# Kernel tuning notes

Measured on AMD Instinct MI355X. Metric: run time of the kernel, lower is better.

The kernel has to match this reference:

```python
import jax, jax.numpy as jnp
import numpy as np

NUM_FREQS = 10
NUM_VOXELS = 512
N_POINTS = 262144
IN_DIM = 3
INPUT_CH = IN_DIM + 2 * NUM_FREQS * IN_DIM  # 63


def posenc(x, num_freqs):
    # NeRF positional encoding: [x, sin(x*2^0), cos(x*2^0), ..., sin(x*2^(F-1)), cos(x*2^(F-1))]
    freqs = (2.0 ** jnp.arange(num_freqs)).astype(x.dtype)           # (F,)
    xf = x[:, None, :] * freqs[None, :, None]                        # (N, F, D)
    sc = jnp.stack([jnp.sin(xf), jnp.cos(xf)], axis=2)               # (N, F, 2, D)
    return jnp.concatenate([x, sc.reshape(x.shape[0], -1)], axis=-1)  # (N, D + 2*F*D)


def setup_inputs() -> dict:
    key = jax.random.key(0)
    k_x, k_w, k_v = jax.random.split(key, 3)
    X = jax.random.normal(k_x, (N_POINTS, IN_DIM), dtype=jnp.float32)
    # linear_mappings reshaped to (3*num_voxels, input_ch), used as Linear weight (no bias)
    W = jax.random.normal(k_w, (3 * NUM_VOXELS, INPUT_CH), dtype=jnp.float32) * 0.02
    row_ids = jnp.arange(N_POINTS, dtype=jnp.int64 if jax.config.jax_enable_x64 else jnp.int32)
    voxel_ids = jax.random.randint(k_v, (N_POINTS,), 0, NUM_VOXELS)
    return {"X": X, "W": W, "row_ids": row_ids, "voxel_ids": voxel_ids}


def reference(X, W, row_ids, voxel_ids):
    encoded_X = posenc(X, NUM_FREQS)                      # (N, 63)
    rgb_clusters = encoded_X @ W.T                        # (N, 3*num_voxels) -- wasteful dense GEMM
    # col_indices per selected row: [3v, 3v+1, 3v+2]
    cols = jnp.stack([3 * voxel_ids, 3 * voxel_ids + 1, 3 * voxel_ids + 2], axis=1)  # (M, 3)
    vals = rgb_clusters[row_ids[:, None], cols]           # (M, 3)
    rgb = jnp.zeros((X.shape[0], 3), dtype=X.dtype)
    rgb = rgb.at[row_ids].set(vals)
    return rgb
```

## Files before the change

### kernel.cpp

```cpp
#include <hip/hip_runtime.h>
#include <math.h>

#define N_POINTS   262144
#define NUM_FREQS  10
#define NUM_VOXELS 512
#define HALF_VOX   256
#define VSTRIDE    200
#define HALF_HALFS (HALF_VOX * VSTRIDE)
#define HALF_F4    (HALF_HALFS / 8)
#define CHUNKS     (HALF_HALFS * 2 / 1024)


typedef _Float16 half2v __attribute__((ext_vector_type(2)));

__device__ __forceinline__ half2v u2h(unsigned int u) {
    union { unsigned int u; half2v h; } c; c.u = u; return c.h;
}

__device__ __forceinline__ float dot2acc(half2v a, half2v b, float acc) {
#if __has_builtin(__builtin_amdgcn_fdot2)
    return __builtin_amdgcn_fdot2(a, b, acc, false);
#else
    return acc + (float)a[0] * (float)b[0] + (float)a[1] * (float)b[1];
#endif
}

__device__ __forceinline__ half2v pkrtz(float a, float b) {
#if __has_builtin(__builtin_amdgcn_cvt_pkrtz)
    auto r = __builtin_amdgcn_cvt_pkrtz(a, b);
    union { decltype(r) r_; half2v h; } c; c.r_ = r; return c.h;
#else
    half2v h; h[0] = (_Float16)a; h[1] = (_Float16)b; return h;
#endif
}

__global__ __launch_bounds__(1024) void pack_w(
    const float* __restrict__ W, _Float16* __restrict__ Wp)
{
    const int g  = blockIdx.x * 1024 + threadIdx.x;
    const int v  = g / 50;
    const int p0 = (g - v * 50) * 4;
    union { _Float16 h[4]; float2 f2; } u;
    #pragma unroll
    for (int j = 0; j < 4; ++j) {
        const int p = p0 + j;
        float val = 0.0f;
        if (p < 192) {
            const int row = p >> 6, col = p & 63;
            if (col != 3) {
                const int wc = col - (col >= 4);
                val = W[v * 189 + row * 63 + wc];
            }
        }
        u.h[j] = (_Float16)val;
    }
    _Float16* dst = Wp + (size_t)(v >> 8) * HALF_HALFS
                       + (size_t)(v & 255) * VSTRIDE + p0;
    *reinterpret_cast<float2*>(dst) = u.f2;
}

__device__ __forceinline__ void stage_async(
    const _Float16* __restrict__ WpHalf, _Float16* lw, int t)
{
#if __has_builtin(__builtin_amdgcn_global_load_lds)
    const int lane = t & 63;
    const int w    = t >> 6;
    const char* src = (const char*)WpHalf + lane * 16;
    char*       dst = (char*)lw;
    #pragma unroll
    for (int c = w; c < 2 * CHUNKS / 2; c += 16) {
        __builtin_amdgcn_global_load_lds(
            (const __attribute__((address_space(1))) void*)(src + (size_t)c * 1024),
            (__attribute__((address_space(3))) void*)(dst + (size_t)c * 1024),
            16, 0, 0);
    }
#else
    const float4* __restrict__ s4 = (const float4*)WpHalf;
    float4* d4 = (float4*)lw;
    for (int j = t; j < HALF_F4; j += 1024) d4[j] = s4[j];
#endif
}

__global__ __launch_bounds__(1024) void voxlin_lds(
    const float* __restrict__ X,
    const _Float16* __restrict__ Wp,
    const int* __restrict__ row_ids,
    const int* __restrict__ voxel_ids,
    float* __restrict__ out)
{
    __shared__ float4 lwv[HALF_F4];
    _Float16* const lw = (_Float16*)lwv;

    const int t = threadIdx.x;
    const int i = blockIdx.x * 1024 + t;

    stage_async(Wp, lw, t);

    const int   v  = voxel_ids[i];
    const float x0 = X[3*i + 0];
    const float x1 = X[3*i + 1];
    const float x2 = X[3*i + 2];
    const int   r  = row_ids[i];

    half2v eh[32];
    eh[0] = pkrtz(x0, x1);
    eh[1] = pkrtz(x2, 0.0f);
    {
        float s0, c0, s1, c1, s2, c2;
        __sincosf(x0, &s0, &c0);
        __sincosf(x1, &s1, &c1);
        __sincosf(x2, &s2, &c2);
        #pragma unroll
        for (int f = 0; f < NUM_FREQS; ++f) {
            const int b = 2 + 3 * f;
            eh[b + 0] = pkrtz(s0, s1);
            eh[b + 1] = pkrtz(s2, c0);
            eh[b + 2] = pkrtz(c1, c2);
            if (f < NUM_FREQS - 1) {
                const float ns0 = 2.0f*s0*c0, nc0 = c0*c0 - s0*s0;
                const float ns1 = 2.0f*s1*c1, nc1 = c1*c1 - s1*s1;
                const float ns2 = 2.0f*s2*c2, nc2 = c2*c2 - s2*s2;
                s0 = ns0; c0 = nc0; s1 = ns1; c1 = nc1; s2 = ns2; c2 = nc2;
            }
        }
    }

    float a0 = 0.0f, a1 = 0.0f, a2 = 0.0f;

    #pragma unroll
    for (int h = 0; h < 2; ++h) {
        if (h == 1) {
            __syncthreads();
            stage_async(Wp + HALF_HALFS, lw, t);
        }
        __syncthreads();

        if ((v >> 8) == h) {
            const uint4* __restrict__ wb =
                (const uint4*)lw + (v & (HALF_VOX - 1)) * (VSTRIDE / 8);
            float acc[3];
            #pragma unroll
            for (int rr = 0; rr < 3; ++rr) {
                float a = 0.0f;
                #pragma unroll
                for (int k = 0; k < 8; ++k) {
                    const uint4 q = wb[rr * 8 + k];
                    a = dot2acc(u2h(q.x), eh[4*k + 0], a);
                    a = dot2acc(u2h(q.y), eh[4*k + 1], a);
                    a = dot2acc(u2h(q.z), eh[4*k + 2], a);
                    a = dot2acc(u2h(q.w), eh[4*k + 3], a);
                }
                acc[rr] = a;
            }
            a0 = acc[0]; a1 = acc[1]; a2 = acc[2];
        }
    }

    out[3*r + 0] = a0;
    out[3*r + 1] = a1;
    out[3*r + 2] = a2;
}

__global__ __launch_bounds__(256) void voxlin_fallback(
    const float* __restrict__ X, const float* __restrict__ W,
    const int* __restrict__ row_ids, const int* __restrict__ voxel_ids,
    float* __restrict__ out)
{
    const int i = blockIdx.x * 256 + threadIdx.x;
    if (i >= N_POINTS) return;
    const float x0 = X[3*i], x1 = X[3*i+1], x2 = X[3*i+2];
    const int v = voxel_ids[i];
    const float* __restrict__ w0 = W + v * 189;
    const float* __restrict__ w1 = w0 + 63;
    const float* __restrict__ w2 = w0 + 126;
    float a0 = x0*w0[0] + x1*w0[1] + x2*w0[2];
    float a1 = x0*w1[0] + x1*w1[1] + x2*w1[2];
    float a2 = x0*w2[0] + x1*w2[1] + x2*w2[2];
    float s0, c0, s1, c1, s2, c2;
    __sincosf(x0, &s0, &c0); __sincosf(x1, &s1, &c1); __sincosf(x2, &s2, &c2);
    #pragma unroll
    for (int f = 0; f < NUM_FREQS; ++f) {
        const int b = 3 + 6*f;
        a0 += s0*w0[b] + s1*w0[b+1] + s2*w0[b+2] + c0*w0[b+3] + c1*w0[b+4] + c2*w0[b+5];
        a1 += s0*w1[b] + s1*w1[b+1] + s2*w1[b+2] + c0*w1[b+3] + c1*w1[b+4] + c2*w1[b+5];
        a2 += s0*w2[b] + s1*w2[b+1] + s2*w2[b+2] + c0*w2[b+3] + c1*w2[b+4] + c2*w2[b+5];
        if (f < NUM_FREQS - 1) {
            const float ns0 = 2.0f*s0*c0, nc0 = c0*c0 - s0*s0;
            const float ns1 = 2.0f*s1*c1, nc1 = c1*c1 - s1*s1;
            const float ns2 = 2.0f*s2*c2, nc2 = c2*c2 - s2*s2;
            s0 = ns0; c0 = nc0; s1 = ns1; c1 = nc1; s2 = ns2; c2 = nc2;
        }
    }
    const int rr = row_ids[i];
    out[3*rr] = a0; out[3*rr+1] = a1; out[3*rr+2] = a2;
}

extern "C" void kernel_launch(void* const* d_in, const int* in_sizes, int n_in,
                              void* d_out, int out_size, void* d_ws, size_t ws_size,
                              hipStream_t stream) {
    const float* X         = (const float*)d_in[0];
    const float* W         = (const float*)d_in[1];
    const int*   row_ids   = (const int*)d_in[2];
    const int*   voxel_ids = (const int*)d_in[3];
    float*       out       = (float*)d_out;

    const size_t need = (size_t)2 * HALF_HALFS * sizeof(_Float16);

    if (ws_size >= need) {
        _Float16* Wp = (_Float16*)d_ws;
        pack_w<<<25, 1024, 0, stream>>>(W, Wp);
        voxlin_lds<<<N_POINTS / 1024, 1024, 0, stream>>>(X, Wp, row_ids,
                                                         voxel_ids, out);
    } else {
        voxlin_fallback<<<(N_POINTS + 255) / 256, 256, 0, stream>>>(
            X, W, row_ids, voxel_ids, out);
    }
}
```

Before: 69.59 us.

## Partition points by voxel half within block to remove wave divergence

Within each block, points are compacted through LDS so that those using the low voxel half come first and those using the high half follow, using a ballot and per-wave prefix counts. Each half's dot-product phase then runs on a contiguous range of threads, so fewer waves execute both phases with half their lanes masked off. Results are un-permuted through LDS before the scattered store. This costs extra LDS traffic and barriers. The pack kernel is also relaunched with 256-thread blocks.

After: 69.36 us. No clear change (-0.3%).

```diff
diff --git a/kernel.cpp b/kernel.cpp
--- a/kernel.cpp
+++ b/kernel.cpp
@@ -34,10 +34,10 @@
 #endif
 }
 
-__global__ __launch_bounds__(1024) void pack_w(
+__global__ __launch_bounds__(256) void pack_w(
     const float* __restrict__ W, _Float16* __restrict__ Wp)
 {
-    const int g  = blockIdx.x * 1024 + threadIdx.x;
+    const int g  = blockIdx.x * 256 + threadIdx.x;
     const int v  = g / 50;
     const int p0 = (g - v * 50) * 4;
     union { _Float16 h[4]; float2 f2; } u;
@@ -68,7 +68,7 @@
     const char* src = (const char*)WpHalf + lane * 16;
     char*       dst = (char*)lw;
     #pragma unroll
-    for (int c = w; c < 2 * CHUNKS / 2; c += 16) {
+    for (int c = w; c < CHUNKS; c += 16) {
         __builtin_amdgcn_global_load_lds(
             (const __attribute__((address_space(1))) void*)(src + (size_t)c * 1024),
             (__attribute__((address_space(3))) void*)(dst + (size_t)c * 1024),
@@ -88,11 +88,15 @@
     const int* __restrict__ voxel_ids,
     float* __restrict__ out)
 {
-    __shared__ float4 lwv[HALF_F4];
+    __shared__ float4    lwv[HALF_F4];
+    __shared__ float4    pts[1024];
+    __shared__ int       wcnt[16];
     _Float16* const lw = (_Float16*)lwv;
 
-    const int t = threadIdx.x;
-    const int i = blockIdx.x * 1024 + t;
+    const int t    = threadIdx.x;
+    const int lane = t & 63;
+    const int wid  = t >> 6;
+    const int i    = blockIdx.x * 1024 + t;
 
     stage_async(Wp, lw, t);
 
@@ -102,14 +106,35 @@
     const float x2 = X[3*i + 2];
     const int   r  = row_ids[i];
 
+    const bool lo = (v < HALF_VOX);
+    const unsigned long long m = __ballot(lo);
+    if (lane == 0) wcnt[wid] = __popcll(m);
+    __syncthreads();
+    int pref_lo = 0, tot_lo = 0;
+    #pragma unroll
+    for (int w = 0; w < 16; ++w) {
+        const int c = wcnt[w];
+        if (w < wid) pref_lo += c;
+        tot_lo += c;
+    }
+    const int mb = __popcll(m & ((1ull << lane) - 1ull));
+    const int mypos = lo ? (pref_lo + mb)
+                         : (tot_lo + 64 * wid - pref_lo + (lane - mb));
+    pts[mypos] = make_float4(x0, x1, x2, __int_as_float(v));
+    const int n0 = tot_lo;
+    __syncthreads();
+
+    const float4 q  = pts[t];
+    const int    sv = __float_as_int(q.w);
+
     half2v eh[32];
-    eh[0] = pkrtz(x0, x1);
-    eh[1] = pkrtz(x2, 0.0f);
+    eh[0] = pkrtz(q.x, q.y);
+    eh[1] = pkrtz(q.z, 0.0f);
     {
         float s0, c0, s1, c1, s2, c2;
-        __sincosf(x0, &s0, &c0);
-        __sincosf(x1, &s1, &c1);
-        __sincosf(x2, &s2, &c2);
+        __sincosf(q.x, &s0, &c0);
+        __sincosf(q.y, &s1, &c1);
+        __sincosf(q.z, &s2, &c2);
         #pragma unroll
         for (int f = 0; f < NUM_FREQS; ++f) {
             const int b = 2 + 3 * f;
@@ -132,23 +157,23 @@
         if (h == 1) {
             __syncthreads();
             stage_async(Wp + HALF_HALFS, lw, t);
-        }
-        __syncthreads();
-
-        if ((v >> 8) == h) {
+            __syncthreads();
+        }
+        const bool active = (h == 0) ? (t < n0) : (t >= n0);
+        if (active) {
             const uint4* __restrict__ wb =
-                (const uint4*)lw + (v & (HALF_VOX - 1)) * (VSTRIDE / 8);
+                (const uint4*)lw + (sv & (HALF_VOX - 1)) * (VSTRIDE / 8);
             float acc[3];
             #pragma unroll
             for (int rr = 0; rr < 3; ++rr) {
                 float a = 0.0f;
                 #pragma unroll
                 for (int k = 0; k < 8; ++k) {
-                    const uint4 q = wb[rr * 8 + k];
-                    a = dot2acc(u2h(q.x), eh[4*k + 0], a);
-                    a = dot2acc(u2h(q.y), eh[4*k + 1], a);
-                    a = dot2acc(u2h(q.z), eh[4*k + 2], a);
-                    a = dot2acc(u2h(q.w), eh[4*k + 3], a);
+                    const uint4 qq = wb[rr * 8 + k];
+                    a = dot2acc(u2h(qq.x), eh[4*k + 0], a);
+                    a = dot2acc(u2h(qq.y), eh[4*k + 1], a);
+                    a = dot2acc(u2h(qq.z), eh[4*k + 2], a);
+                    a = dot2acc(u2h(qq.w), eh[4*k + 3], a);
                 }
                 acc[rr] = a;
             }
@@ -156,9 +181,13 @@
         }
     }
 
-    out[3*r + 0] = a0;
-    out[3*r + 1] = a1;
-    out[3*r + 2] = a2;
+    __syncthreads();
+    pts[t] = make_float4(a0, a1, a2, 0.0f);
+    __syncthreads();
+    const float4 res = pts[mypos];
+    out[3*r + 0] = res.x;
+    out[3*r + 1] = res.y;
+    out[3*r + 2] = res.z;
 }
 
 __global__ __launch_bounds__(256) void voxlin_fallback(
@@ -208,7 +237,7 @@
 
     if (ws_size >= need) {
         _Float16* Wp = (_Float16*)d_ws;
-        pack_w<<<25, 1024, 0, stream>>>(W, Wp);
+        pack_w<<<100, 256, 0, stream>>>(W, Wp);
         voxlin_lds<<<N_POINTS / 1024, 1024, 0, stream>>>(X, Wp, row_ids,
                                                          voxel_ids, out);
     } else {
```
